# Optimization experiments

Hardware: AMD Instinct MI355X
Metric: run time of the kernel (lower is better)

The kernel has to match this reference:

```python
import jax, jax.numpy as jnp
import numpy as np

WS = (2, 7, 7)      # window_size (D,H,W)
SS = (1, 3, 3)      # shift_size
HEADS = 3
EPS = 1e-5


def _window_partition(x, ws):
    B, D, H, W, C = x.shape
    x = x.reshape(B, D // ws[0], ws[0], H // ws[1], ws[1], W // ws[2], ws[2], C)
    x = x.transpose(0, 1, 3, 5, 2, 4, 6, 7)
    return x.reshape(-1, ws[0] * ws[1] * ws[2], C)


def _window_reverse(w, ws, dims):
    B, D, H, W = dims
    x = w.reshape(B, D // ws[0], H // ws[1], W // ws[2], ws[0], ws[1], ws[2], -1)
    x = x.transpose(0, 1, 4, 2, 5, 3, 6, 7)
    return x.reshape(B, D, H, W, -1)


def _ln(x, g, b):
    m = x.mean(-1, keepdims=True)
    v = x.var(-1, keepdims=True)
    return (x - m) / jnp.sqrt(v + EPS) * g + b


def setup_inputs() -> dict:
    key = jax.random.key(0)
    ks = jax.random.split(key, 6)
    B, D, H, W, C = 2, 32, 56, 56, 96
    hid = 4 * C
    x = jax.random.normal(ks[0], (B, D, H, W, C), jnp.float32)
    # shifted-window attention mask (Video-Swin compute_mask), no padding needed here
    img = np.zeros((1, D, H, W, 1), np.float32)
    cnt = 0
    for d in (slice(0, -WS[0]), slice(-WS[0], -SS[0]), slice(-SS[0], None)):
        for h in (slice(0, -WS[1]), slice(-WS[1], -SS[1]), slice(-SS[1], None)):
            for w in (slice(0, -WS[2]), slice(-WS[2], -SS[2]), slice(-SS[2], None)):
                img[:, d, h, w, :] = cnt
                cnt += 1
    mw = _window_partition(img, WS).reshape(-1, WS[0] * WS[1] * WS[2])  # (nW, N)
    diff = mw[:, None, :] - mw[:, :, None]
    mask = jnp.asarray(np.where(diff != 0, -100.0, 0.0).astype(np.float32))
    s = 0.02
    return {
        "x": x,
        "mask_matrix": mask,
        "norm1_g": jnp.ones((C,), jnp.float32),
        "norm1_b": jnp.zeros((C,), jnp.float32),
        "qkv_w": s * jax.random.normal(ks[1], (3 * C, C), jnp.float32),
        "qkv_b": jnp.zeros((3 * C,), jnp.float32),
        "proj_w": s * jax.random.normal(ks[2], (C, C), jnp.float32),
        "proj_b": jnp.zeros((C,), jnp.float32),
        "norm2_g": jnp.ones((C,), jnp.float32),
        "norm2_b": jnp.zeros((C,), jnp.float32),
        "fc1_w": s * jax.random.normal(ks[3], (hid, C), jnp.float32),
        "fc1_b": jnp.zeros((hid,), jnp.float32),
        "fc2_w": s * jax.random.normal(ks[4], (C, hid), jnp.float32),
        "fc2_b": jnp.zeros((C,), jnp.float32),
    }


def reference(x, mask_matrix, norm1_g, norm1_b, qkv_w, qkv_b, proj_w, proj_b,
              norm2_g, norm2_b, fc1_w, fc1_b, fc2_w, fc2_b):
    B, D, H, W, C = x.shape
    hd = C // HEADS
    scale = hd ** -0.5
    shortcut = x
    # part1: norm -> shift -> window attention -> unshift
    h1 = _ln(x, norm1_g, norm1_b)
    sx = jnp.roll(h1, (-SS[0], -SS[1], -SS[2]), axis=(1, 2, 3))
    xw = _window_partition(sx, WS)              # (B_, N, C)
    Bw, N, _ = xw.shape
    qkv = xw @ qkv_w.T + qkv_b                  # (B_, N, 3C)
    qkv = qkv.reshape(Bw, N, 3, HEADS, hd).transpose(2, 0, 3, 1, 4)
    q, k, v = qkv[0] * scale, qkv[1], qkv[2]    # (B_, h, N, hd)
    attn = jnp.einsum('bhnd,bhmd->bhnm', q, k)
    nW = mask_matrix.shape[0]
    attn = attn.reshape(Bw // nW, nW, HEADS, N, N) + mask_matrix[None, :, None]
    attn = jax.nn.softmax(attn.reshape(Bw, HEADS, N, N), axis=-1)
    o = jnp.einsum('bhnm,bhmd->bhnd', attn, v).transpose(0, 2, 1, 3).reshape(Bw, N, C)
    o = o @ proj_w.T + proj_b
    o = _window_reverse(o, WS, (B, D, H, W))
    o = jnp.roll(o, SS, axis=(1, 2, 3))
    x = shortcut + o
    # part2: MLP with residual
    h2 = _ln(x, norm2_g, norm2_b)
    x = x + (jax.nn.gelu(h2 @ fc1_w.T + fc1_b, approximate=False) @ fc2_w.T + fc2_b)
    return x
```

## Files before the change

### kernel.cpp

```cpp
#include <hip/hip_runtime.h>
#include <hip/hip_bf16.h>

#define NTOK   200704
#define NWIN   2048
#define NT     98
#define CCH    96
#define HID    384

typedef __attribute__((ext_vector_type(8))) short bf16x8;
typedef __attribute__((ext_vector_type(4))) short s16x4;
typedef __attribute__((ext_vector_type(4))) float f32x4;
typedef __attribute__((ext_vector_type(4))) int   i32x4;

#define MFMA(a, b, c) __builtin_amdgcn_mfma_f32_16x16x32_bf16((a), (b), (c), 0, 0, 0)

__device__ __forceinline__ float bf2f(__hip_bfloat16 v) { return __bfloat162float(v); }

__device__ __forceinline__ short f2bf_s(float v) {
  __hip_bfloat16 h = __float2bfloat16(v);
  return *reinterpret_cast<short*>(&h);
}

__device__ __forceinline__ unsigned pack2(float a, float b) {
  unsigned ua = (unsigned short)f2bf_s(a);
  unsigned ub = (unsigned short)f2bf_s(b);
  return ua | (ub << 16);
}

__device__ __forceinline__ float gelu_f(float v) {
  float u = v * (1.5957691216057308f + 0.0713548162726f * v * v);
  return __fdividef(v, 1.f + __expf(-u));
}

__global__ __launch_bounds__(256) void k0_cvt(
    const float* __restrict__ w1, const float* __restrict__ w2,
    const float* __restrict__ qkvw, const float* __restrict__ pw,
    __hip_bfloat16* __restrict__ w1b, __hip_bfloat16* __restrict__ w2b,
    __hip_bfloat16* __restrict__ qkvwb, __hip_bfloat16* __restrict__ pwb) {
  int i = blockIdx.x * 256 + threadIdx.x;
  if (i < HID * CCH) {
    w1b[i] = __float2bfloat16(w1[i]);
    w2b[i] = __float2bfloat16(w2[i]);
  }
  if (i < 3 * CCH * CCH) qkvwb[i] = __float2bfloat16(qkvw[i]);
  if (i < CCH * CCH)     pwb[i]   = __float2bfloat16(pw[i]);
}

__global__ __launch_bounds__(256) void k1_ln_window(
    const float* __restrict__ x, const float* __restrict__ g,
    const float* __restrict__ bt, __hip_bfloat16* __restrict__ xw) {
  int token = blockIdx.x * 8 + (threadIdx.x >> 5);
  int lane = threadIdx.x & 31;
  if (token >= NTOK) return;
  int wb = token / NT;
  int n  = token - wb * NT;
  int b = wb >> 10;
  int rem = wb & 1023;
  int wd = rem >> 6, wh = (rem >> 3) & 7, ww = rem & 7;
  int id = n / 49, ih = (n / 7) % 7, iw = n % 7;
  int dd = wd * 2 + id + 1; if (dd >= 32) dd -= 32;
  int hh = wh * 7 + ih + 3; if (hh >= 56) hh -= 56;
  int w2 = ww * 7 + iw + 3; if (w2 >= 56) w2 -= 56;
  const float* src = x + ((((size_t)b * 32 + dd) * 56 + hh) * 56 + w2) * CCH;
  float v0 = src[lane], v1 = src[lane + 32], v2 = src[lane + 64];
  float s = v0 + v1 + v2, ss = v0 * v0 + v1 * v1 + v2 * v2;
  #pragma unroll
  for (int off = 16; off; off >>= 1) {
    s  += __shfl_xor(s,  off, 32);
    ss += __shfl_xor(ss, off, 32);
  }
  float m   = s * (1.f / 96.f);
  float inv = rsqrtf(ss * (1.f / 96.f) - m * m + 1e-5f);
  __hip_bfloat16* dst = xw + (size_t)token * CCH;
  dst[lane]      = __float2bfloat16((v0 - m) * inv * g[lane]      + bt[lane]);
  dst[lane + 32] = __float2bfloat16((v1 - m) * inv * g[lane + 32] + bt[lane + 32]);
  dst[lane + 64] = __float2bfloat16((v2 - m) * inv * g[lane + 64] + bt[lane + 64]);
}

#define QK_S 40
#define VT_S 120
__global__ __launch_bounds__(256, 4) void k2_attn(
    const __hip_bfloat16* __restrict__ xw, const __hip_bfloat16* __restrict__ qkvwb,
    const float* __restrict__ qkv_b, __hip_bfloat16* __restrict__ obuf) {
  __shared__ __align__(16) __hip_bfloat16 Qs[112 * QK_S];
  __shared__ __align__(16) __hip_bfloat16 Ks[112 * QK_S];
  __shared__ __align__(16) __hip_bfloat16 Vts[32 * VT_S];
  __shared__ unsigned char ridL[112];
  int bid = blockIdx.x, tid = threadIdx.x;
  int wb = bid / 3, h = bid - wb * 3;
  int wid = tid >> 6, lane = tid & 63, lr = lane & 15, lq = lane >> 4;
  int mw = wb & 1023;
  int wd = mw >> 6, wh = (mw >> 3) & 7, ww = mw & 7;
  bool hasmask = (wd == 15) || (wh == 7) || (ww == 7);
  const __hip_bfloat16* xp = xw + (size_t)wb * (NT * CCH);
  int h32 = h * 32;

  if (tid < 112) {
    int n = tid < NT ? tid : NT - 1;
    int id = n / 49, r2 = n - id * 49, ih = r2 / 7, iw = r2 - ih * 7;
    int ud = wd * 2 + id, uh = wh * 7 + ih, uw = ww * 7 + iw;
    int dr = (ud < 30) ? 0 : (ud == 30 ? 1 : 2);
    int hr = (uh < 49) ? 0 : (uh < 53 ? 1 : 2);
    int wr = (uw < 49) ? 0 : (uw < 53 ? 1 : 2);
    ridL[tid] = (unsigned char)(dr * 9 + hr * 3 + wr);
  }

  for (int job = wid; job < 42; job += 4) {
    int mt = job / 6, ct = job - (job / 6) * 6;
    int tok = mt * 16 + lr;
    int tokc = tok < NT ? tok : NT - 1;
    const __hip_bfloat16* xrow = xp + (size_t)tokc * CCH;
    bf16x8 xf0 = *(const bf16x8*)(xrow + lq * 8);
    bf16x8 xf1 = *(const bf16x8*)(xrow + 32 + lq * 8);
    bf16x8 xf2 = *(const bf16x8*)(xrow + 64 + lq * 8);
    if (ct < 4) {
      int which = ct >> 1;
      int grow0 = which * CCH + h32 + (ct & 1) * 16;
      const __hip_bfloat16* wr0 = qkvwb + (size_t)(grow0 + lr) * CCH;
      f32x4 acc = *(const f32x4*)&qkv_b[grow0 + lq * 4];
      acc = MFMA(*(const bf16x8*)(wr0 + lq * 8),      xf0, acc);
      acc = MFMA(*(const bf16x8*)(wr0 + 32 + lq * 8), xf1, acc);
      acc = MFMA(*(const bf16x8*)(wr0 + 64 + lq * 8), xf2, acc);
      if (which == 0) {
        #pragma unroll
        for (int r = 0; r < 4; ++r) acc[r] *= 0.17677669529663689f;
      }
      s16x4 pk4;
      #pragma unroll
      for (int r = 0; r < 4; ++r) pk4[r] = f2bf_s(acc[r]);
      __hip_bfloat16* dst = (which == 0) ? Qs : Ks;
      *(s16x4*)&dst[tok * QK_S + (ct & 1) * 16 + lq * 4] = pk4;
    } else {
      int dt = ct & 1;
      int vrow = 2 * CCH + h32 + dt * 16 + lr;
      const __hip_bfloat16* wv = qkvwb + (size_t)vrow * CCH;
      float bv = qkv_b[vrow];
      f32x4 acc = {bv, bv, bv, bv};
      acc = MFMA(xf0, *(const bf16x8*)(wv + lq * 8),      acc);
      acc = MFMA(xf1, *(const bf16x8*)(wv + 32 + lq * 8), acc);
      acc = MFMA(xf2, *(const bf16x8*)(wv + 64 + lq * 8), acc);
      s16x4 pk4;
      #pragma unroll
      for (int r = 0; r < 4; ++r) pk4[r] = f2bf_s(acc[r]);
      *(s16x4*)&Vts[(dt * 16 + lr) * VT_S + mt * 16 + lq * 4] = pk4;
    }
  }
  __syncthreads();

  for (int mt = wid; mt < 7; mt += 4) {
    bf16x8 qf = *(const bf16x8*)&Qs[(mt * 16 + lr) * QK_S + lq * 8];
    f32x4 s[7];
    #pragma unroll
    for (int nt = 0; nt < 7; ++nt) s[nt] = {0.f, 0.f, 0.f, 0.f};
    #pragma unroll
    for (int nt = 0; nt < 7; ++nt) {
      bf16x8 kf = *(const bf16x8*)&Ks[(nt * 16 + lr) * QK_S + lq * 8];
      s[nt] = MFMA(kf, qf, s[nt]);
    }
    if (hasmask) {
      int rq = ridL[mt * 16 + lr];
      #pragma unroll
      for (int nt = 0; nt < 7; ++nt)
        #pragma unroll
        for (int r = 0; r < 4; ++r)
          s[nt][r] += (ridL[nt * 16 + lq * 4 + r] != rq) ? -100.f : 0.f;
    }
    #pragma unroll
    for (int r = 0; r < 4; ++r)
      s[6][r] = (lq * 4 + r >= 2) ? -1e30f : s[6][r];
    float m = s[0][0];
    #pragma unroll
    for (int nt = 0; nt < 7; ++nt)
      #pragma unroll
      for (int r = 0; r < 4; ++r) m = fmaxf(m, s[nt][r]);
    m = fmaxf(m, __shfl_xor(m, 16));
    m = fmaxf(m, __shfl_xor(m, 32));
    float sum = 0.f;
    #pragma unroll
    for (int nt = 0; nt < 7; ++nt)
      #pragma unroll
      for (int r = 0; r < 4; ++r) {
        float e = __expf(s[nt][r] - m);
        s[nt][r] = e;
        sum += e;
      }
    sum += __shfl_xor(sum, 16);
    sum += __shfl_xor(sum, 32);
    float inv = 1.f / sum;
    #pragma unroll
    for (int nt = 0; nt < 7; ++nt)
      #pragma unroll
      for (int r = 0; r < 4; ++r) s[nt][r] *= inv;
    unsigned pk[6][2];
    #pragma unroll
    for (int nt = 0; nt < 6; ++nt) {
      pk[nt][0] = pack2(s[nt][0], s[nt][1]);
      pk[nt][1] = pack2(s[nt][2], s[nt][3]);
    }
    f32x4 o0 = {0.f, 0.f, 0.f, 0.f}, o1 = {0.f, 0.f, 0.f, 0.f};
    int srcA = lr + ((lq & 1) << 5);
    bool hi = (lq & 2) != 0;
    #pragma unroll
    for (int ks = 0; ks < 3; ++ks) {
      int a0 = __shfl((int)pk[2 * ks][0], srcA);
      int b0 = __shfl((int)pk[2 * ks + 1][0], srcA);
      int a1 = __shfl((int)pk[2 * ks][1], srcA);
      int b1 = __shfl((int)pk[2 * ks + 1][1], srcA);
      int a2 = __shfl((int)pk[2 * ks][0], srcA + 16);
      int b2 = __shfl((int)pk[2 * ks + 1][0], srcA + 16);
      int a3 = __shfl((int)pk[2 * ks][1], srcA + 16);
      int b3 = __shfl((int)pk[2 * ks + 1][1], srcA + 16);
      i32x4 wv4;
      wv4[0] = hi ? b0 : a0;
      wv4[1] = hi ? b1 : a1;
      wv4[2] = hi ? b2 : a2;
      wv4[3] = hi ? b3 : a3;
      bf16x8 pf = __builtin_bit_cast(bf16x8, wv4);
      o0 = MFMA(*(const bf16x8*)&Vts[lr * VT_S + ks * 32 + lq * 8], pf, o0);
      o1 = MFMA(*(const bf16x8*)&Vts[(16 + lr) * VT_S + ks * 32 + lq * 8], pf, o1);
    }
    float p96 = __shfl(s[6][0], lr);
    float p97 = __shfl(s[6][1], lr);
    #pragma unroll
    for (int r = 0; r < 4; ++r) {
      int d0 = lq * 4 + r, d1 = 16 + lq * 4 + r;
      o0[r] += p96 * bf2f(Vts[d0 * VT_S + 96]) + p97 * bf2f(Vts[d0 * VT_S + 97]);
      o1[r] += p96 * bf2f(Vts[d1 * VT_S + 96]) + p97 * bf2f(Vts[d1 * VT_S + 97]);
    }
    int q = mt * 16 + lr;
    if (q < NT) {
      __hip_bfloat16* ob = obuf + ((size_t)wb * NT + q) * CCH + h32;
      s16x4 w0, w1;
      #pragma unroll
      for (int r = 0; r < 4; ++r) { w0[r] = f2bf_s(o0[r]); w1[r] = f2bf_s(o1[r]); }
      *(s16x4*)(ob + lq * 4) = w0;
      *(s16x4*)(ob + 16 + lq * 4) = w1;
    }
  }
}

#define XS_S 104
__global__ __launch_bounds__(256) void k3_proj(
    const __hip_bfloat16* __restrict__ obuf, const float* __restrict__ x,
    const __hip_bfloat16* __restrict__ pwb, const float* __restrict__ pb,
    float* __restrict__ out) {
  __shared__ __align__(16) __hip_bfloat16 os[112 * XS_S];
  int wb = blockIdx.x, tid = threadIdx.x;
  int wid = tid >> 6, lane = tid & 63, lr = lane & 15, lq = lane >> 4;
  const __hip_bfloat16* src = obuf + (size_t)wb * (NT * CCH);
  for (int q = tid; q < 112 * 12; q += 256) {
    int n = q / 12, g = q - n * 12;
    bf16x8 v = {0, 0, 0, 0, 0, 0, 0, 0};
    if (n < NT) v = *(const bf16x8*)(src + n * CCH + g * 8);
    *(bf16x8*)&os[n * XS_S + g * 8] = v;
  }
  __syncthreads();
  int b = wb >> 10, rem = wb & 1023;
  int wd = rem >> 6, wh = (rem >> 3) & 7, ww = rem & 7;
  for (int job = wid; job < 42; job += 4) {
    int mt = job / 6, ct = job - (job / 6) * 6;
    float bv = pb[ct * 16 + lr];
    f32x4 acc = {bv, bv, bv, bv};
    const __hip_bfloat16* wrow = pwb + (size_t)(ct * 16 + lr) * CCH;
    #pragma unroll
    for (int ks = 0; ks < 3; ++ks) {
      bf16x8 a = *(const bf16x8*)&os[(mt * 16 + lr) * XS_S + ks * 32 + lq * 8];
      bf16x8 bw = *(const bf16x8*)(wrow + ks * 32 + lq * 8);
      acc = MFMA(a, bw, acc);
    }
    #pragma unroll
    for (int r = 0; r < 4; ++r) {
      int token = mt * 16 + lq * 4 + r;
      if (token < NT) {
        int id = token / 49, r2 = token - id * 49;
        int ih = r2 / 7, iw = r2 - ih * 7;
        int dd = wd * 2 + id + 1; if (dd >= 32) dd -= 32;
        int hh = wh * 7 + ih + 3; if (hh >= 56) hh -= 56;
        int w2 = ww * 7 + iw + 3; if (w2 >= 56) w2 -= 56;
        size_t gi = ((((size_t)b * 32 + dd) * 56 + hh) * 56 + w2) * CCH + ct * 16 + lr;
        out[gi] = x[gi] + acc[r];
      }
    }
  }
}

#define XB_S 104
__global__ __launch_bounds__(256, 5) void k4_mlp(
    float* __restrict__ io, const float* __restrict__ g, const float* __restrict__ bt,
    const __hip_bfloat16* __restrict__ w1b, const float* __restrict__ b1,
    const __hip_bfloat16* __restrict__ w2b, const float* __restrict__ b2) {
  __shared__ __align__(16) __hip_bfloat16 Xb[32 * XB_S];
  __shared__ __align__(16) __hip_bfloat16 Ht[32 * 384];
  int tid = threadIdx.x;
  size_t base = (size_t)blockIdx.x * 32 * CCH;
  {
    int grp = tid >> 5, lane = tid & 31;
    #pragma unroll
    for (int t0 = 0; t0 < 4; ++t0) {
      int t = grp + t0 * 8;
      const float* src = io + base + (size_t)t * CCH;
      float v0 = src[lane], v1 = src[lane + 32], v2 = src[lane + 64];
      float s = v0 + v1 + v2, ss = v0 * v0 + v1 * v1 + v2 * v2;
      #pragma unroll
      for (int off = 16; off; off >>= 1) {
        s  += __shfl_xor(s,  off, 32);
        ss += __shfl_xor(ss, off, 32);
      }
      float m   = s * (1.f / 96.f);
      float inv = rsqrtf(ss * (1.f / 96.f) - m * m + 1e-5f);
      Xb[t * XB_S + lane]      = __float2bfloat16((v0 - m) * inv * g[lane]      + bt[lane]);
      Xb[t * XB_S + lane + 32] = __float2bfloat16((v1 - m) * inv * g[lane + 32] + bt[lane + 32]);
      Xb[t * XB_S + lane + 64] = __float2bfloat16((v2 - m) * inv * g[lane + 64] + bt[lane + 64]);
    }
  }
  __syncthreads();
  int wid = tid >> 6, lane = tid & 63, lr = lane & 15, lq = lane >> 4;
  {
    bf16x8 xb[2][3];
    #pragma unroll
    for (int tt = 0; tt < 2; ++tt)
      #pragma unroll
      for (int ks = 0; ks < 3; ++ks)
        xb[tt][ks] = *(const bf16x8*)&Xb[(tt * 16 + lr) * XB_S + ks * 32 + lq * 8];
    f32x4 acc[2][6];
    #pragma unroll
    for (int nt = 0; nt < 6; ++nt) {
      f32x4 bv = *(const f32x4*)&b1[96 * wid + 16 * nt + 4 * lq];
      acc[0][nt] = bv;
      acc[1][nt] = bv;
    }
    const __hip_bfloat16* wrow = w1b + (size_t)(96 * wid + lr) * CCH;
    #pragma unroll
    for (int nt = 0; nt < 6; ++nt) {
      #pragma unroll
      for (int ks = 0; ks < 3; ++ks) {
        bf16x8 a = *(const bf16x8*)(wrow + (size_t)(16 * nt) * CCH + ks * 32 + lq * 8);
        acc[0][nt] = MFMA(a, xb[0][ks], acc[0][nt]);
        acc[1][nt] = MFMA(a, xb[1][ks], acc[1][nt]);
      }
    }
    #pragma unroll
    for (int tt = 0; tt < 2; ++tt) {
      int row = tt * 16 + lr;
      char* hb = (char*)Ht + row * 768;
      int sw = (row & 7) << 4;
      #pragma unroll
      for (int nt = 0; nt < 6; ++nt) {
        s16x4 pk;
        #pragma unroll
        for (int r = 0; r < 4; ++r) pk[r] = f2bf_s(gelu_f(acc[tt][nt][r]));
        *(s16x4*)(hb + ((192 * wid + 32 * nt + 8 * lq) ^ sw)) = pk;
      }
    }
  }
  __syncthreads();
  {
    int tt = wid >> 1, ntb = (wid & 1) * 3;
    f32x4 acc2[3];
    #pragma unroll
    for (int j = 0; j < 3; ++j) {
      float bv = b2[16 * (ntb + j) + lr];
      acc2[j] = {bv, bv, bv, bv};
    }
    const char* hb = (const char*)Ht + (tt * 16 + lr) * 768;
    int sw = (lr & 7) << 4;
    #pragma unroll 4
    for (int kk = 0; kk < 12; ++kk) {
      bf16x8 a = *(const bf16x8*)(hb + ((64 * kk + 16 * lq) ^ sw));
      #pragma unroll
      for (int j = 0; j < 3; ++j) {
        bf16x8 b = *(const bf16x8*)&w2b[(size_t)(16 * (ntb + j) + lr) * HID + kk * 32 + lq * 8];
        acc2[j] = MFMA(a, b, acc2[j]);
      }
    }
    #pragma unroll
    for (int j = 0; j < 3; ++j)
      #pragma unroll
      for (int r = 0; r < 4; ++r) {
        size_t gi = base + (size_t)(tt * 16 + lq * 4 + r) * CCH + 16 * (ntb + j) + lr;
        io[gi] = io[gi] + acc2[j][r];
      }
  }
}

extern "C" void kernel_launch(void* const* d_in, const int* in_sizes, int n_in,
                              void* d_out, int out_size, void* d_ws, size_t ws_size,
                              hipStream_t stream) {
  const float* x    = (const float*)d_in[0];
  const float* n1g  = (const float*)d_in[2];
  const float* n1b  = (const float*)d_in[3];
  const float* qkvw = (const float*)d_in[4];
  const float* qkvb = (const float*)d_in[5];
  const float* pw   = (const float*)d_in[6];
  const float* pb   = (const float*)d_in[7];
  const float* n2g  = (const float*)d_in[8];
  const float* n2b  = (const float*)d_in[9];
  const float* w1   = (const float*)d_in[10];
  const float* b1   = (const float*)d_in[11];
  const float* w2   = (const float*)d_in[12];
  const float* b2   = (const float*)d_in[13];
  float* out = (float*)d_out;

  __hip_bfloat16* xw    = (__hip_bfloat16*)d_ws;
  __hip_bfloat16* obuf  = xw + (size_t)NTOK * CCH;
  __hip_bfloat16* w1b   = obuf + (size_t)NTOK * CCH;
  __hip_bfloat16* w2b   = w1b + HID * CCH;
  __hip_bfloat16* qkvwb = w2b + HID * CCH;
  __hip_bfloat16* pwb   = qkvwb + 3 * CCH * CCH;

  k0_cvt<<<(HID * CCH + 255) / 256, 256, 0, stream>>>(w1, w2, qkvw, pw, w1b, w2b, qkvwb, pwb);
  k1_ln_window<<<NTOK / 8, 256, 0, stream>>>(x, n1g, n1b, xw);
  k2_attn<<<NWIN * 3, 256, 0, stream>>>(xw, qkvwb, qkvb, obuf);
  k3_proj<<<NWIN, 256, 0, stream>>>(obuf, x, pwb, pb, out);
  k4_mlp<<<NTOK / 32, 256, 0, stream>>>(out, n2g, n2b, w1b, b1, w2b, b2);
}
```

Before: 482.2 us.

## Keep MLP hidden activations in registers via lane shuffles and transpose proj MFMA

The MLP kernel now gives each wave its own 16 tokens (64 per block) and computes fc1 in two halves. The GELU outputs are packed to bf16 and redistributed with cross-lane shuffles so they can feed fc2 MFMAs directly, which removes the shared-memory hidden buffer and a block barrier. Both the proj and MLP kernels swap MFMA operand order so each lane holds four contiguous channels, allowing vectorized float4 residual loads and stores. The cost is more registers per wave (12 accumulators plus 6 output accumulators), the removal of the occupancy hint, and halving the block count of the MLP launch.

```diff
diff --git a/kernel.cpp b/kernel.cpp
--- a/kernel.cpp
+++ b/kernel.cpp
@@ -10,6 +10,7 @@
 typedef __attribute__((ext_vector_type(8))) short bf16x8;
 typedef __attribute__((ext_vector_type(4))) short s16x4;
 typedef __attribute__((ext_vector_type(4))) float f32x4;
+typedef __attribute__((ext_vector_type(2))) float f32x2;
 typedef __attribute__((ext_vector_type(4))) int   i32x4;
 
 #define MFMA(a, b, c) __builtin_amdgcn_mfma_f32_16x16x32_bf16((a), (b), (c), 0, 0, 0)
@@ -259,44 +260,40 @@
   int wd = rem >> 6, wh = (rem >> 3) & 7, ww = rem & 7;
   for (int job = wid; job < 42; job += 4) {
     int mt = job / 6, ct = job - (job / 6) * 6;
-    float bv = pb[ct * 16 + lr];
-    f32x4 acc = {bv, bv, bv, bv};
+    f32x4 acc = *(const f32x4*)&pb[ct * 16 + lq * 4];
     const __hip_bfloat16* wrow = pwb + (size_t)(ct * 16 + lr) * CCH;
     #pragma unroll
     for (int ks = 0; ks < 3; ++ks) {
-      bf16x8 a = *(const bf16x8*)&os[(mt * 16 + lr) * XS_S + ks * 32 + lq * 8];
-      bf16x8 bw = *(const bf16x8*)(wrow + ks * 32 + lq * 8);
-      acc = MFMA(a, bw, acc);
-    }
-    #pragma unroll
-    for (int r = 0; r < 4; ++r) {
-      int token = mt * 16 + lq * 4 + r;
-      if (token < NT) {
-        int id = token / 49, r2 = token - id * 49;
-        int ih = r2 / 7, iw = r2 - ih * 7;
-        int dd = wd * 2 + id + 1; if (dd >= 32) dd -= 32;
-        int hh = wh * 7 + ih + 3; if (hh >= 56) hh -= 56;
-        int w2 = ww * 7 + iw + 3; if (w2 >= 56) w2 -= 56;
-        size_t gi = ((((size_t)b * 32 + dd) * 56 + hh) * 56 + w2) * CCH + ct * 16 + lr;
-        out[gi] = x[gi] + acc[r];
-      }
+      bf16x8 osf = *(const bf16x8*)&os[(mt * 16 + lr) * XS_S + ks * 32 + lq * 8];
+      bf16x8 wf  = *(const bf16x8*)(wrow + ks * 32 + lq * 8);
+      acc = MFMA(wf, osf, acc);
+    }
+    int token = mt * 16 + lr;
+    if (token < NT) {
+      int id = token / 49, r2 = token - id * 49;
+      int ih = r2 / 7, iw = r2 - ih * 7;
+      int dd = wd * 2 + id + 1; if (dd >= 32) dd -= 32;
+      int hh = wh * 7 + ih + 3; if (hh >= 56) hh -= 56;
+      int w2 = ww * 7 + iw + 3; if (w2 >= 56) w2 -= 56;
+      size_t gi = ((((size_t)b * 32 + dd) * 56 + hh) * 56 + w2) * CCH + ct * 16 + lq * 4;
+      f32x4 xv = *(const f32x4*)&x[gi];
+      *(f32x4*)&out[gi] = xv + acc;
     }
   }
 }
 
 #define XB_S 104
-__global__ __launch_bounds__(256, 5) void k4_mlp(
+__global__ __launch_bounds__(256) void k4_mlp(
     float* __restrict__ io, const float* __restrict__ g, const float* __restrict__ bt,
     const __hip_bfloat16* __restrict__ w1b, const float* __restrict__ b1,
     const __hip_bfloat16* __restrict__ w2b, const float* __restrict__ b2) {
-  __shared__ __align__(16) __hip_bfloat16 Xb[32 * XB_S];
-  __shared__ __align__(16) __hip_bfloat16 Ht[32 * 384];
+  __shared__ __align__(16) __hip_bfloat16 Xb[64 * XB_S];
   int tid = threadIdx.x;
-  size_t base = (size_t)blockIdx.x * 32 * CCH;
+  size_t base = (size_t)blockIdx.x * 64 * CCH;
   {
     int grp = tid >> 5, lane = tid & 31;
     #pragma unroll
-    for (int t0 = 0; t0 < 4; ++t0) {
+    for (int t0 = 0; t0 < 8; ++t0) {
       int t = grp + t0 * 8;
       const float* src = io + base + (size_t)t * CCH;
       float v0 = src[lane], v1 = src[lane + 32], v2 = src[lane + 64];
@@ -315,71 +312,69 @@
   }
   __syncthreads();
   int wid = tid >> 6, lane = tid & 63, lr = lane & 15, lq = lane >> 4;
+  bf16x8 xb[3];
+  #pragma unroll
+  for (int ks = 0; ks < 3; ++ks)
+    xb[ks] = *(const bf16x8*)&Xb[(wid * 16 + lr) * XB_S + ks * 32 + lq * 8];
+  f32x4 acc2[6];
+  #pragma unroll
+  for (int ct = 0; ct < 6; ++ct)
+    acc2[ct] = *(const f32x4*)&b2[ct * 16 + lq * 4];
+  int srcA = ((lq & 1) << 5) + lr;
+  bool hiSel = (lq & 2) != 0;
+  #pragma unroll
+  for (int h = 0; h < 2; ++h) {
+    f32x4 acc[12];
+    #pragma unroll
+    for (int nt = 0; nt < 12; ++nt)
+      acc[nt] = *(const f32x4*)&b1[(h * 12 + nt) * 16 + lq * 4];
+    #pragma unroll
+    for (int nt = 0; nt < 12; ++nt) {
+      const __hip_bfloat16* wrow = w1b + (size_t)((h * 12 + nt) * 16 + lr) * CCH;
+      #pragma unroll
+      for (int ks = 0; ks < 3; ++ks) {
+        bf16x8 wf = *(const bf16x8*)(wrow + ks * 32 + lq * 8);
+        acc[nt] = MFMA(wf, xb[ks], acc[nt]);
+      }
+    }
+    unsigned u[12][2];
+    #pragma unroll
+    for (int nt = 0; nt < 12; ++nt) {
+      u[nt][0] = pack2(gelu_f(acc[nt][0]), gelu_f(acc[nt][1]));
+      u[nt][1] = pack2(gelu_f(acc[nt][2]), gelu_f(acc[nt][3]));
+    }
+    #pragma unroll
+    for (int kk = 0; kk < 6; ++kk) {
+      int A0 = __shfl((int)u[2 * kk][0], srcA);
+      int B0 = __shfl((int)u[2 * kk + 1][0], srcA);
+      int A1 = __shfl((int)u[2 * kk][1], srcA);
+      int B1 = __shfl((int)u[2 * kk + 1][1], srcA);
+      int A2 = __shfl((int)u[2 * kk][0], srcA + 16);
+      int B2 = __shfl((int)u[2 * kk + 1][0], srcA + 16);
+      int A3 = __shfl((int)u[2 * kk][1], srcA + 16);
+      int B3 = __shfl((int)u[2 * kk + 1][1], srcA + 16);
+      i32x4 wv;
+      wv[0] = hiSel ? B0 : A0;
+      wv[1] = hiSel ? B1 : A1;
+      wv[2] = hiSel ? B2 : A2;
+      wv[3] = hiSel ? B3 : A3;
+      bf16x8 pa = __builtin_bit_cast(bf16x8, wv);
+      int kkg = h * 6 + kk;
+      #pragma unroll
+      for (int ct = 0; ct < 6; ++ct) {
+        bf16x8 wf = *(const bf16x8*)&w2b[(size_t)(ct * 16 + lr) * HID + kkg * 32 + lq * 8];
+        acc2[ct] = MFMA(wf, pa, acc2[ct]);
+      }
+    }
+  }
   {
-    bf16x8 xb[2][3];
-    #pragma unroll
-    for (int tt = 0; tt < 2; ++tt)
-      #pragma unroll
-      for (int ks = 0; ks < 3; ++ks)
-        xb[tt][ks] = *(const bf16x8*)&Xb[(tt * 16 + lr) * XB_S + ks * 32 + lq * 8];
-    f32x4 acc[2][6];
-    #pragma unroll
-    for (int nt = 0; nt < 6; ++nt) {
-      f32x4 bv = *(const f32x4*)&b1[96 * wid + 16 * nt + 4 * lq];
-      acc[0][nt] = bv;
-      acc[1][nt] = bv;
-    }
-    const __hip_bfloat16* wrow = w1b + (size_t)(96 * wid + lr) * CCH;
-    #pragma unroll
-    for (int nt = 0; nt < 6; ++nt) {
-      #pragma unroll
-      for (int ks = 0; ks < 3; ++ks) {
-        bf16x8 a = *(const bf16x8*)(wrow + (size_t)(16 * nt) * CCH + ks * 32 + lq * 8);
-        acc[0][nt] = MFMA(a, xb[0][ks], acc[0][nt]);
-        acc[1][nt] = MFMA(a, xb[1][ks], acc[1][nt]);
-      }
-    }
-    #pragma unroll
-    for (int tt = 0; tt < 2; ++tt) {
-      int row = tt * 16 + lr;
-      char* hb = (char*)Ht + row * 768;
-      int sw = (row & 7) << 4;
-      #pragma unroll
-      for (int nt = 0; nt < 6; ++nt) {
-        s16x4 pk;
-        #pragma unroll
-        for (int r = 0; r < 4; ++r) pk[r] = f2bf_s(gelu_f(acc[tt][nt][r]));
-        *(s16x4*)(hb + ((192 * wid + 32 * nt + 8 * lq) ^ sw)) = pk;
-      }
-    }
-  }
-  __syncthreads();
-  {
-    int tt = wid >> 1, ntb = (wid & 1) * 3;
-    f32x4 acc2[3];
-    #pragma unroll
-    for (int j = 0; j < 3; ++j) {
-      float bv = b2[16 * (ntb + j) + lr];
-      acc2[j] = {bv, bv, bv, bv};
-    }
-    const char* hb = (const char*)Ht + (tt * 16 + lr) * 768;
-    int sw = (lr & 7) << 4;
-    #pragma unroll 4
-    for (int kk = 0; kk < 12; ++kk) {
-      bf16x8 a = *(const bf16x8*)(hb + ((64 * kk + 16 * lq) ^ sw));
-      #pragma unroll
-      for (int j = 0; j < 3; ++j) {
-        bf16x8 b = *(const bf16x8*)&w2b[(size_t)(16 * (ntb + j) + lr) * HID + kk * 32 + lq * 8];
-        acc2[j] = MFMA(a, b, acc2[j]);
-      }
-    }
-    #pragma unroll
-    for (int j = 0; j < 3; ++j)
-      #pragma unroll
-      for (int r = 0; r < 4; ++r) {
-        size_t gi = base + (size_t)(tt * 16 + lq * 4 + r) * CCH + 16 * (ntb + j) + lr;
-        io[gi] = io[gi] + acc2[j][r];
-      }
+    float* orow = io + base + (size_t)(wid * 16 + lr) * CCH;
+    #pragma unroll
+    for (int ct = 0; ct < 6; ++ct) {
+      int ch0 = ct * 16 + lq * 4;
+      f32x4 cur = *(const f32x4*)(orow + ch0);
+      *(f32x4*)(orow + ch0) = cur + acc2[ct];
+    }
   }
 }
 
@@ -412,5 +407,5 @@
   k1_ln_window<<<NTOK / 8, 256, 0, stream>>>(x, n1g, n1b, xw);
   k2_attn<<<NWIN * 3, 256, 0, stream>>>(xw, qkvwb, qkvb, obuf);
   k3_proj<<<NWIN, 256, 0, stream>>>(obuf, x, pwb, pb, out);
-  k4_mlp<<<NTOK / 32, 256, 0, stream>>>(out, n2g, n2b, w1b, b1, w2b, b2);
-}
+  k4_mlp<<<NTOK / 64, 256, 0, stream>>>(out, n2g, n2b, w1b, b1, w2b, b2);
+}
```

Result: slower. 509.1 us (+5.6%).
